# Kernel optimization log

Measured on AMD Instinct MI355X. Metric: run time of the kernel, lower is better.

The kernel has to match this reference:

```python
import jax, jax.numpy as jnp
import numpy as np

EMB = 2048
NQH = 16          # num_q_heads
G = 4             # group_size
NKV = NQH // G    # 4 kv heads
HD = EMB // NQH   # 128 head_dim
B, S = 2, 2048


def setup_inputs() -> dict:
    key = jax.random.key(0)
    ks = jax.random.split(key, 6)
    scale = 1.0 / np.sqrt(EMB)
    x = jax.random.normal(ks[0], (B, S, EMB), dtype=jnp.float32)
    attn_mask = jnp.zeros((B, S), dtype=bool)  # unused placeholder
    # torch Linear weights: (out_features, in_features)
    Wq = jax.random.normal(ks[1], (EMB, EMB), dtype=jnp.float32) * scale
    Wk = jax.random.normal(ks[2], (EMB // G, EMB), dtype=jnp.float32) * scale
    Wv = jax.random.normal(ks[3], (EMB // G, EMB), dtype=jnp.float32) * scale
    Wo = jax.random.normal(ks[4], (EMB, EMB), dtype=jnp.float32) * scale
    return {"x": x, "attn_mask": attn_mask, "is_causal": 1,
            "Wq": Wq, "Wk": Wk, "Wv": Wv, "Wo": Wo}


def reference(x, attn_mask, is_causal, Wq, Wk, Wv, Wo):
    b, n, _ = x.shape
    q = x @ Wq.T                      # (b, n, EMB)
    k = x @ Wk.T                      # (b, n, EMB//G)
    v = x @ Wv.T                      # (b, n, EMB//G)
    # q: b n (h_full d) -> b h_full n d, then (h g) split with h=NKV outer
    q = q.reshape(b, n, NQH, HD).transpose(0, 2, 1, 3)      # (b, NQH, n, d)
    q = q.reshape(b, NKV, G, n, HD).transpose(0, 2, 1, 3, 4)  # (b, g, h, n, d)
    k = k.reshape(b, n, NKV, HD).transpose(0, 2, 1, 3)      # (b, h, s, d)
    v = v.reshape(b, n, NKV, HD).transpose(0, 2, 1, 3)      # (b, h, s, d)
    attn = jnp.einsum('bghnd,bhsd->bghns', q, k) / np.sqrt(HD)
    scores = jax.nn.softmax(attn, axis=-1)  # dropout p=0.0 -> identity
    out = jnp.einsum('bghns,bhsd->bghnd', scores, v)        # (b, g, h, n, d)
    # b g h n d -> b n (h g) d -> b n (h g d)
    out = out.transpose(0, 3, 2, 1, 4).reshape(b, n, EMB)
    y = out @ Wo.T
    return y
```

## Files before the change

### kernel.cpp

```cpp
#include <hip/hip_runtime.h>
#include <stdint.h>


typedef short s8v __attribute__((ext_vector_type(8)));
typedef float f4  __attribute__((ext_vector_type(4)));
typedef unsigned short u16;

#define GLD_LDS(g, l) __builtin_amdgcn_global_load_lds(                     \
    (const __attribute__((address_space(1))) void*)(g),                     \
    (__attribute__((address_space(3))) void*)(l), 16, 0, 0)

__device__ __forceinline__ u16 f2bf(float f) {
    union { float f; uint32_t u; } v; v.f = f;
    uint32_t u = v.u;
    return (u16)((u + 0x7fffu + ((u >> 16) & 1u)) >> 16);
}

__device__ __forceinline__ float fexp2(float x) {
#if __has_builtin(__builtin_amdgcn_exp2f)
    return __builtin_amdgcn_exp2f(x);
#else
    return exp2f(x);
#endif
}

__global__ void cvt_all(const float* __restrict__ x,  const float* __restrict__ wq,
                        const float* __restrict__ wk, const float* __restrict__ wv,
                        const float* __restrict__ wo_,
                        u16* __restrict__ xb, u16* __restrict__ wqkv,
                        u16* __restrict__ wob)
{
    int i = blockIdx.x * blockDim.x + threadIdx.x;
    const float4* s; ushort4* d; int so, dofs;
    if (i < 2097152)      { s = (const float4*)x;   d = (ushort4*)xb;   so = i;           dofs = so; }
    else if (i < 3145728) { s = (const float4*)wq;  d = (ushort4*)wqkv; so = i - 2097152; dofs = so; }
    else if (i < 3407872) { s = (const float4*)wk;  d = (ushort4*)wqkv; so = i - 3145728; dofs = so + 1048576; }
    else if (i < 3670016) { s = (const float4*)wv;  d = (ushort4*)wqkv; so = i - 3407872; dofs = so + 1310720; }
    else                  { s = (const float4*)wo_; d = (ushort4*)wob;  so = i - 3670016; dofs = so; }
    float4 v = s[so];
    ushort4 o;
    o.x = f2bf(v.x); o.y = f2bf(v.y); o.z = f2bf(v.z); o.w = f2bf(v.w);
    d[dofs] = o;
}

template<int MODE>
__global__ __launch_bounds__(512, 2)
void gemm256(const u16* __restrict__ A, const u16* __restrict__ Bm,
             int M, int N, int K,
             u16* __restrict__ qkOut, u16* __restrict__ vtOut,
             float* __restrict__ fOut)
{
    __shared__ __attribute__((aligned(16))) u16 lds[2][2][2][8192];

    const int tid  = threadIdx.x;
    const int lane = tid & 63, quad = lane >> 4, l16 = lane & 15;
    const int wave = tid >> 6;
    const int wr = wave >> 2, wc = wave & 3;

    int bx, by;
    {
        const int nwgx = gridDim.x;
        const int nwg  = nwgx * gridDim.y;
        const int flat = blockIdx.y * nwgx + blockIdx.x;
        const int nflat = (flat & 7) * (nwg >> 3) + (flat >> 3);
        bx = nflat % nwgx; by = nflat / nwgx;
    }
    const int m0 = by * 256, n0 = bx * 256;
    const int NT = K >> 6;

    f4 acc[8][4] = {};

#define VMC6() asm volatile("s_waitcnt vmcnt(6)" ::: "memory")
#define VMC0() asm volatile("s_waitcnt vmcnt(0)" ::: "memory")
#define BAR()  __builtin_amdgcn_s_barrier()

#define STG(bf, op, h, t) if ((t) < NT) {                                   \
        const u16* gb = (op) ? Bm : A;                                      \
        const int rb = ((op) ? n0 : m0) + (h) * 128;                        \
        _Pragma("unroll")                                                   \
        for (int j = 0; j < 2; j++) {                                       \
            int s_ = j * 512 + tid;                                         \
            int r_ = s_ >> 3, cc = s_ & 7;                                  \
            GLD_LDS(gb + (size_t)(rb + r_) * K + (t) * 64                   \
                       + ((cc ^ (r_ & 7)) << 3),                            \
                    &lds[bf][op][h][(j * 512 + (tid & ~63)) * 8]);          \
        } }

#define RD_A(bf, qm, ar) {                                                  \
        _Pragma("unroll")                                                   \
        for (int f = 0; f < 4; f++) {                                       \
            int r_ = (qm) * 64 + f * 16 + l16;                              \
            _Pragma("unroll")                                               \
            for (int kc = 0; kc < 2; kc++)                                  \
                ar[f][kc] = *(const s8v*)(&lds[bf][0][wr]                   \
                    [r_ * 64 + (((kc * 4 + quad) ^ (r_ & 7)) << 3)]);       \
        } }

#define RD_B(bf, qn, br) {                                                  \
        _Pragma("unroll")                                                   \
        for (int f = 0; f < 2; f++) {                                       \
            int r_ = (wc & 1) * 64 + ((qn) * 2 + f) * 16 + l16;             \
            _Pragma("unroll")                                               \
            for (int kc = 0; kc < 2; kc++)                                  \
                br[f][kc] = *(const s8v*)(&lds[bf][1][wc >> 1]              \
                    [r_ * 64 + (((kc * 4 + quad) ^ (r_ & 7)) << 3)]);       \
        } }

#define MM(qm, qn, ar, br) {                                                \
        __builtin_amdgcn_s_setprio(1);                                      \
        _Pragma("unroll")                                                   \
        for (int f = 0; f < 4; f++)                                         \
            _Pragma("unroll")                                               \
            for (int g = 0; g < 2; g++) {                                   \
                acc[(qm)*4+f][(qn)*2+g] = __builtin_amdgcn_mfma_f32_16x16x32_bf16( \
                    ar[f][0], br[g][0], acc[(qm)*4+f][(qn)*2+g], 0, 0, 0);  \
                acc[(qm)*4+f][(qn)*2+g] = __builtin_amdgcn_mfma_f32_16x16x32_bf16( \
                    ar[f][1], br[g][1], acc[(qm)*4+f][(qn)*2+g], 0, 0, 0);  \
            }                                                               \
        __builtin_amdgcn_s_setprio(0); }

    STG(0,1,0,0); STG(0,1,1,0); STG(0,0,0,0); STG(0,0,1,0);
    STG(1,1,0,1); STG(1,1,1,1); STG(1,0,0,1);
    VMC6(); BAR();

    for (int T = 0; T < NT; T += 2) {
        const bool more = (T + 2 < NT);
        s8v a0[4][2], a1[4][2], b0[2][2], b1[2][2];
        RD_A(0,0,a0); RD_B(0,0,b0);
        STG(1,0,1,T+1);
        BAR(); MM(0,0,a0,b0); BAR();
        RD_B(0,1,b1);
        BAR(); MM(0,1,a0,b1); BAR();
        RD_A(0,1,a1);
        STG(0,1,0,T+2);
        BAR(); MM(1,0,a1,b0); BAR();
        STG(0,1,1,T+2); STG(0,0,0,T+2);
        BAR(); MM(1,1,a1,b1);
        if (more) { VMC6(); } else { VMC0(); }
        BAR();
        RD_A(1,0,a0); RD_B(1,0,b0);
        STG(0,0,1,T+2);
        BAR(); MM(0,0,a0,b0); BAR();
        RD_B(1,1,b1);
        BAR(); MM(0,1,a0,b1); BAR();
        RD_A(1,1,a1);
        STG(1,1,0,T+3);
        BAR(); MM(1,0,a1,b0); BAR();
        STG(1,1,1,T+3); STG(1,0,0,T+3);
        BAR(); MM(1,1,a1,b1);
        if (more) { VMC6(); } else { VMC0(); }
        BAR();
    }
#undef STG
#undef RD_A
#undef RD_B
#undef MM

    if (MODE == 0) {
        if (n0 < 2560) {
            const float qs = (n0 < 2048)
                ? (0.08838834764831845f * 1.4426950408889634f) : 1.0f;
            #pragma unroll
            for (int mi = 0; mi < 8; mi++) {
                int gm0 = m0 + wr * 128 + mi * 16 + quad * 4;
                #pragma unroll
                for (int ni = 0; ni < 4; ni++) {
                    int gn = n0 + wc * 64 + ni * 16 + l16;
                    #pragma unroll
                    for (int r = 0; r < 4; r++)
                        qkOut[(size_t)(gm0 + r) * 2560 + gn] = f2bf(acc[mi][ni][r] * qs);
                }
            }
        } else {
            #pragma unroll
            for (int mi = 0; mi < 8; mi++) {
                int gm0 = m0 + wr * 128 + mi * 16 + quad * 4;
                int bb = gm0 >> 11, s = gm0 & 2047;
                #pragma unroll
                for (int ni = 0; ni < 4; ni++) {
                    int gn = n0 + wc * 64 + ni * 16 + l16;
                    int dd = gn - 2560;
                    ushort4 pk;
                    pk.x = f2bf(acc[mi][ni][0]); pk.y = f2bf(acc[mi][ni][1]);
                    pk.z = f2bf(acc[mi][ni][2]); pk.w = f2bf(acc[mi][ni][3]);
                    *(ushort4*)(vtOut +
                        ((size_t)(bb * 4 + (dd >> 7)) * 128 + (dd & 127)) * 2048 + s) = pk;
                }
            }
        }
    } else {
        #pragma unroll
        for (int mi = 0; mi < 8; mi++) {
            int gm0 = m0 + wr * 128 + mi * 16 + quad * 4;
            #pragma unroll
            for (int ni = 0; ni < 4; ni++) {
                int gn = n0 + wc * 64 + ni * 16 + l16;
                #pragma unroll
                for (int r = 0; r < 4; r++)
                    fOut[(size_t)(gm0 + r) * N + gn] = acc[mi][ni][r];
            }
        }
    }
#undef VMC6
#undef VMC0
#undef BAR
}

__global__ __launch_bounds__(512, 2)
void attn_kernel(const u16* __restrict__ qk, const u16* __restrict__ vt,
                 u16* __restrict__ ao)
{
    __shared__ __attribute__((aligned(16))) u16 Kb[2][64 * 128];
    __shared__ __attribute__((aligned(16))) u16 Vb[2][128 * 64];
    __shared__ __attribute__((aligned(16))) u16 Ps[8][32 * 72];

    const int tid  = threadIdx.x;
    const int wave = tid >> 6, lane = tid & 63;
    const int quad = lane >> 4, l16 = lane & 15;
    const int bh = blockIdx.x;
    const int b = bh >> 2, h = bh & 3;
    const int hh = wave >> 1, mh = wave & 1;
    const int hq = h * 4 + hh;
    const int qs0 = blockIdx.y * 64;

    s8v aq[2][4];
    #pragma unroll
    for (int mt = 0; mt < 2; mt++) {
        const u16* qrow = qk + (size_t)(b * 2048 + qs0 + (mh * 2 + mt) * 16 + l16) * 2560
                             + hq * 128 + quad * 8;
        #pragma unroll
        for (int c4 = 0; c4 < 4; c4++) aq[mt][c4] = *(const s8v*)(qrow + c4 * 32);
    }

    s8v ones;
    #pragma unroll
    for (int j = 0; j < 8; j++) ones[j] = (short)0x3F80;

    f4 o[2][9] = {};

    const u16* kbase = qk + (size_t)(b * 2048) * 2560 + 2048 + h * 128;
    const u16* vbase = vt + (size_t)bh * 128 * 2048;
    u16* Pw = &Ps[wave][0];

    int bkb[4], bvb[2];
    #pragma unroll
    for (int c4 = 0; c4 < 4; c4++)
        bkb[c4] = l16 * 128 + (((c4 * 4 + quad) ^ (l16 & 7)) * 8);
    #pragma unroll
    for (int kc = 0; kc < 2; kc++)
        bvb[kc] = l16 * 64 + (((kc * 4 + quad) ^ (l16 & 7)) * 8);
    const int apb = l16 * 72 + quad * 8;
    const int pwb = quad * 4 * 72 + l16;

#define STAGE(CUR, S) {                                                       \
        _Pragma("unroll")                                                     \
        for (int i = 0; i < 2; i++) {                                         \
            const int c = wave + i * 8;                                       \
            int kr = c * 4 + (lane >> 4);                                     \
            int ksw = (lane & 15) ^ (kr & 7);                                 \
            GLD_LDS(kbase + (size_t)((S) + kr) * 2560 + ksw * 8,              \
                    &Kb[CUR][c * 512]);                                       \
            int vd = c * 8 + (lane >> 3);                                     \
            int vsw = (lane & 7) ^ (vd & 7);                                  \
            GLD_LDS(vbase + (size_t)vd * 2048 + (S) + vsw * 8,                \
                    &Vb[CUR][c * 512]);                                       \
        } }

#define STEP(CUR, S) {                                                        \
        __syncthreads();    \
        if ((S) + 64 < 2048) STAGE((CUR) ^ 1, (S) + 64);                      \
        s8v bk[4][4];                                                         \
        _Pragma("unroll")                                                     \
        for (int c4 = 0; c4 < 4; c4++)                                        \
            _Pragma("unroll")                                                 \
            for (int cg = 0; cg < 4; cg++)                                    \
                bk[c4][cg] = *(const s8v*)(&Kb[CUR][bkb[c4] + cg * 2048]);    \
        _Pragma("unroll")                                                     \
        for (int mt = 0; mt < 2; mt++) {                                      \
            f4 sc[4] = {};                                                    \
            _Pragma("unroll")                                                 \
            for (int c4 = 0; c4 < 4; c4++)                                    \
                _Pragma("unroll")                                             \
                for (int cg = 0; cg < 4; cg++)                                \
                    sc[cg] = __builtin_amdgcn_mfma_f32_16x16x32_bf16(         \
                        aq[mt][c4], bk[c4][cg], sc[cg], 0, 0, 0);             \
              \
            _Pragma("unroll")                                                 \
            for (int cg = 0; cg < 4; cg++)                                    \
                _Pragma("unroll")                                             \
                for (int r = 0; r < 4; r++)                                   \
                    Pw[pwb + mt * 1152 + r * 72 + cg * 16] =                  \
                        (u16)(__float_as_uint(fexp2(sc[cg][r])) >> 16);       \
        }                                                                     \
        s8v ap[2][2];                                                         \
        _Pragma("unroll")                                                     \
        for (int mt = 0; mt < 2; mt++)                                        \
            _Pragma("unroll")                                                 \
            for (int kc = 0; kc < 2; kc++)                                    \
                ap[mt][kc] = *(const s8v*)(Pw + apb + mt * 1152 + kc * 32);   \
        _Pragma("unroll")                                                     \
        for (int ch = 0; ch < 8; ch++) {                                      \
            s8v bv0 = *(const s8v*)(&Vb[CUR][bvb[0] + ch * 1024]);            \
            s8v bv1 = *(const s8v*)(&Vb[CUR][bvb[1] + ch * 1024]);            \
            _Pragma("unroll")                                                 \
            for (int mt = 0; mt < 2; mt++) {                                  \
                o[mt][ch] = __builtin_amdgcn_mfma_f32_16x16x32_bf16(          \
                    ap[mt][0], bv0, o[mt][ch], 0, 0, 0);                      \
                o[mt][ch] = __builtin_amdgcn_mfma_f32_16x16x32_bf16(          \
                    ap[mt][1], bv1, o[mt][ch], 0, 0, 0);                      \
            }                                                                 \
        }                                                                     \
        _Pragma("unroll")                                                     \
        for (int mt = 0; mt < 2; mt++) {                                      \
            o[mt][8] = __builtin_amdgcn_mfma_f32_16x16x32_bf16(               \
                ap[mt][0], ones, o[mt][8], 0, 0, 0);                          \
            o[mt][8] = __builtin_amdgcn_mfma_f32_16x16x32_bf16(               \
                ap[mt][1], ones, o[mt][8], 0, 0, 0);                          \
        } }

    STAGE(0, 0);
    for (int s0 = 0; s0 < 2048; s0 += 128) {
        STEP(0, s0);
        STEP(1, s0 + 64);
    }
#undef STEP
#undef STAGE

    #pragma unroll
    for (int mt = 0; mt < 2; mt++)
        #pragma unroll
        for (int r = 0; r < 4; r++) {
            float inv = 1.f / o[mt][8][r];
            int gm = b * 2048 + qs0 + (mh * 2 + mt) * 16 + quad * 4 + r;
            #pragma unroll
            for (int ch = 0; ch < 8; ch++)
                ao[(size_t)gm * 2048 + hq * 128 + ch * 16 + l16] =
                    f2bf(o[mt][ch][r] * inv);
        }
}

extern "C" void kernel_launch(void* const* d_in, const int* in_sizes, int n_in,
                              void* d_out, int out_size, void* d_ws, size_t ws_size,
                              hipStream_t stream)
{
    const float* x  = (const float*)d_in[0];
    const float* Wq = (const float*)d_in[3];
    const float* Wk = (const float*)d_in[4];
    const float* Wv = (const float*)d_in[5];
    const float* Wo = (const float*)d_in[6];

    char* ws = (char*)d_ws;
    u16* xb   = (u16*)(ws);
    u16* wqkv = (u16*)(ws + 16777216);
    u16* wo   = (u16*)(ws + 29360128);
    u16* qkb  = (u16*)(ws + 37748736);
    u16* vtb  = (u16*)(ws + 58720256);
    u16* ao   = (u16*)(ws + 62914560);
    if (ws_size < 79691776u) return;

    cvt_all<<<18432, 256, 0, stream>>>(x, Wq, Wk, Wv, Wo, xb, wqkv, wo);

    gemm256<0><<<dim3(12, 16), 512, 0, stream>>>(xb, wqkv, 4096, 3072, 2048,
                                                 qkb, vtb, nullptr);
    attn_kernel<<<dim3(8, 32), 512, 0, stream>>>(qkb, vtb, ao);
    gemm256<1><<<dim3(8, 16), 512, 0, stream>>>(ao, wo, 4096, 2048, 2048,
                                                nullptr, nullptr, (float*)d_out);
}
```

Baseline: 308.8 us.

## Add 256x128 output-projection GEMM and vectorize P stores in attention

```diff
diff --git a/kernel.cpp b/kernel.cpp
--- a/kernel.cpp
+++ b/kernel.cpp
@@ -206,6 +206,124 @@
 #undef BAR
 }
 
+__global__ __launch_bounds__(512, 1)
+void gemm256x128(const u16* __restrict__ A, const u16* __restrict__ Bm,
+                 int M, int N, int K, float* __restrict__ fOut)
+{
+    __shared__ __attribute__((aligned(16))) u16 lds[2][3][8192];
+
+    const int tid  = threadIdx.x;
+    const int lane = tid & 63, quad = lane >> 4, l16 = lane & 15;
+    const int wave = tid >> 6;
+    const int wr = wave >> 2, wc = wave & 3;
+
+    int bx, by;
+    {
+        const int nwgx = gridDim.x;
+        const int nwg  = nwgx * gridDim.y;
+        const int flat = blockIdx.y * nwgx + blockIdx.x;
+        const int nflat = (flat & 7) * (nwg >> 3) + (flat >> 3);
+        bx = nflat % nwgx; by = nflat / nwgx;
+    }
+    const int m0 = by * 256, n0 = bx * 128;
+    const int NT = K >> 6;
+
+    f4 acc[8][2] = {};
+
+#define VMC2() asm volatile("s_waitcnt vmcnt(2)" ::: "memory")
+#define VMC0() asm volatile("s_waitcnt vmcnt(0)" ::: "memory")
+#define BAR()  __builtin_amdgcn_s_barrier()
+
+#define STG(bf, u, t) if ((t) < NT) {                                       \
+        const u16* gb = ((u) == 2) ? Bm : A;                                \
+        const int rb = ((u) == 2) ? n0 : (m0 + (u) * 128);                  \
+        _Pragma("unroll")                                                   \
+        for (int j = 0; j < 2; j++) {                                       \
+            int s_ = j * 512 + tid;                                         \
+            int r_ = s_ >> 3, cc = s_ & 7;                                  \
+            GLD_LDS(gb + (size_t)(rb + r_) * K + (t) * 64                   \
+                       + ((cc ^ (r_ & 7)) << 3),                            \
+                    &lds[bf][u][(j * 512 + (tid & ~63)) * 8]);              \
+        } }
+
+#define RD_A(bf, qm, ar) {                                                  \
+        _Pragma("unroll")                                                   \
+        for (int f = 0; f < 4; f++) {                                       \
+            int r_ = (qm) * 64 + f * 16 + l16;                              \
+            _Pragma("unroll")                                               \
+            for (int kc = 0; kc < 2; kc++)                                  \
+                ar[f][kc] = *(const s8v*)(&lds[bf][wr]                      \
+                    [r_ * 64 + (((kc * 4 + quad) ^ (r_ & 7)) << 3)]);       \
+        } }
+
+#define RD_B(bf, br) {                                                      \
+        _Pragma("unroll")                                                   \
+        for (int f = 0; f < 2; f++) {                                       \
+            int r_ = wc * 32 + f * 16 + l16;                                \
+            _Pragma("unroll")                                               \
+            for (int kc = 0; kc < 2; kc++)                                  \
+                br[f][kc] = *(const s8v*)(&lds[bf][2]                       \
+                    [r_ * 64 + (((kc * 4 + quad) ^ (r_ & 7)) << 3)]);       \
+        } }
+
+#define MM(qm, ar, br) {                                                    \
+        __builtin_amdgcn_s_setprio(1);                                      \
+        _Pragma("unroll")                                                   \
+        for (int f = 0; f < 4; f++)                                         \
+            _Pragma("unroll")                                               \
+            for (int g = 0; g < 2; g++) {                                   \
+                acc[(qm)*4+f][g] = __builtin_amdgcn_mfma_f32_16x16x32_bf16( \
+                    ar[f][0], br[g][0], acc[(qm)*4+f][g], 0, 0, 0);         \
+                acc[(qm)*4+f][g] = __builtin_amdgcn_mfma_f32_16x16x32_bf16( \
+                    ar[f][1], br[g][1], acc[(qm)*4+f][g], 0, 0, 0);         \
+            }                                                               \
+        __builtin_amdgcn_s_setprio(0); }
+
+    STG(0,0,0); STG(0,1,0); STG(0,2,0);
+    STG(1,2,1);
+    VMC2(); BAR();
+
+    for (int T = 0; T < NT; T += 2) {
+        const bool more = (T + 2 < NT);
+        s8v a0[4][2], a1[4][2], b[2][2];
+        RD_A(0,0,a0); RD_B(0,b);
+        STG(1,0,T+1); STG(1,1,T+1);
+        BAR(); MM(0,a0,b); BAR();
+        RD_A(0,1,a1);
+        STG(0,2,T+2);
+        BAR(); MM(1,a1,b);
+        if (more) { VMC2(); } else { VMC0(); }
+        BAR();
+        RD_A(1,0,a0); RD_B(1,b);
+        STG(0,0,T+2); STG(0,1,T+2);
+        BAR(); MM(0,a0,b); BAR();
+        RD_A(1,1,a1);
+        STG(1,2,T+3);
+        BAR(); MM(1,a1,b);
+        if (more) { VMC2(); } else { VMC0(); }
+        BAR();
+    }
+#undef STG
+#undef RD_A
+#undef RD_B
+#undef MM
+#undef VMC2
+#undef VMC0
+#undef BAR
+
+    #pragma unroll
+    for (int mi = 0; mi < 8; mi++) {
+        int gm0 = m0 + wr * 128 + mi * 16 + quad * 4;
+        #pragma unroll
+        for (int ni = 0; ni < 2; ni++) {
+            int gn = n0 + wc * 32 + ni * 16 + l16;
+            #pragma unroll
+            for (int r = 0; r < 4; r++)
+                fOut[(size_t)(gm0 + r) * N + gn] = acc[mi][ni][r];
+        }
+    }
+}
+
 __global__ __launch_bounds__(512, 2)
 void attn_kernel(const u16* __restrict__ qk, const u16* __restrict__ vt,
                  u16* __restrict__ ao)
@@ -250,7 +368,7 @@
     for (int kc = 0; kc < 2; kc++)
         bvb[kc] = l16 * 64 + (((kc * 4 + quad) ^ (l16 & 7)) * 8);
     const int apb = l16 * 72 + quad * 8;
-    const int pwb = quad * 4 * 72 + l16;
+    const int psw = l16 * 72 + quad * 4;
 
 #define STAGE(CUR, S) {                                                       \
         _Pragma("unroll")                                                     \
@@ -283,14 +401,17 @@
                 _Pragma("unroll")                                             \
                 for (int cg = 0; cg < 4; cg++)                                \
                     sc[cg] = __builtin_amdgcn_mfma_f32_16x16x32_bf16(         \
-                        aq[mt][c4], bk[c4][cg], sc[cg], 0, 0, 0);             \
-              \
+                        bk[c4][cg], aq[mt][c4], sc[cg], 0, 0, 0);             \
+               \
             _Pragma("unroll")                                                 \
-            for (int cg = 0; cg < 4; cg++)                                    \
-                _Pragma("unroll")                                             \
-                for (int r = 0; r < 4; r++)                                   \
-                    Pw[pwb + mt * 1152 + r * 72 + cg * 16] =                  \
-                        (u16)(__float_as_uint(fexp2(sc[cg][r])) >> 16);       \
+            for (int cg = 0; cg < 4; cg++) {                                  \
+                ushort4 pk;                                                   \
+                pk.x = (u16)(__float_as_uint(fexp2(sc[cg][0])) >> 16);        \
+                pk.y = (u16)(__float_as_uint(fexp2(sc[cg][1])) >> 16);        \
+                pk.z = (u16)(__float_as_uint(fexp2(sc[cg][2])) >> 16);        \
+                pk.w = (u16)(__float_as_uint(fexp2(sc[cg][3])) >> 16);        \
+                *(ushort4*)(Pw + psw + mt * 1152 + cg * 16) = pk;             \
+            }                                                                 \
         }                                                                     \
         s8v ap[2][2];                                                         \
         _Pragma("unroll")                                                     \
@@ -363,6 +484,6 @@
     gemm256<0><<<dim3(12, 16), 512, 0, stream>>>(xb, wqkv, 4096, 3072, 2048,
                                                  qkb, vtb, nullptr);
     attn_kernel<<<dim3(8, 32), 512, 0, stream>>>(qkb, vtb, ao);
-    gemm256<1><<<dim3(8, 16), 512, 0, stream>>>(ao, wo, 4096, 2048, 2048,
-                                                nullptr, nullptr, (float*)d_out);
-}
+    gemm256x128<<<dim3(16, 16), 512, 0, stream>>>(ao, wo, 4096, 2048, 2048,
+                                                  (float*)d_out);
+}
```

Measured after the change: 282.0 us. -8.7%, faster.
